# Kernel optimization log

Hardware: AMD Instinct MI355X
Metric: run time of the kernel (lower is better)

Reference implementation:

```python
import jax, jax.numpy as jnp
import numpy as np

D, FF, E, K = 1024, 1024, 8, 2  # d_model, ffn_dim, n_experts, top_k
B, S = 4, 1024


def _gelu(x):
    # torch F.gelu default is the exact erf form
    return jax.nn.gelu(x, approximate=False)


def setup_inputs() -> dict:
    key = jax.random.key(0)
    ks = jax.random.split(key, 12)
    s = 0.02
    return {
        "x": jax.random.normal(ks[0], (B, S, D), jnp.float32),
        "gate_w": jax.random.normal(ks[1], (D, E), jnp.float32) * s,
        "gate_b": jnp.zeros((E,), jnp.float32),
        # shared expert (n_shared = 1)
        "sw1": jax.random.normal(ks[2], (D, FF), jnp.float32) * s,
        "sb1": jnp.zeros((FF,), jnp.float32),
        "sw2": jax.random.normal(ks[3], (FF, D), jnp.float32) * s,
        "sb2": jnp.zeros((D,), jnp.float32),
        # routed experts, stacked over E
        "w1": jax.random.normal(ks[4], (E, D, FF), jnp.float32) * s,
        "b1": jnp.zeros((E, FF), jnp.float32),
        "w2": jax.random.normal(ks[5], (E, FF, D), jnp.float32) * s,
        "b2": jnp.zeros((E, D), jnp.float32),
    }


def reference(x, gate_w, gate_b, sw1, sb1, sw2, sb2, w1, b1, w2, b2):
    Bb, Ss, Dm = x.shape
    t = x.reshape(-1, Dm)  # [T, D]
    T = t.shape[0]

    # shared expert(s)
    shared = _gelu(t @ sw1 + sb1) @ sw2 + sb2  # [T, D]

    # gating: softmax over experts, then top-k
    probs = jax.nn.softmax(t @ gate_w + gate_b, axis=-1)  # [T, E]
    topk_p, topk_i = jax.lax.top_k(probs, K)  # [T, K]

    # combine weights: sparse [T, E] with top-k probs (top_k indices are distinct)
    combine = jnp.zeros((T, E), t.dtype).at[
        jnp.arange(T)[:, None], topk_i
    ].set(topk_p)

    # expert FFNs computed densely, combined with sparse routing weights;
    # mathematically identical to the masked gather-GEMM-scatter loop
    h = _gelu(jnp.einsum("td,edf->etf", t, w1) + b1[:, None, :])  # [E, T, FF]
    y = jnp.einsum("etf,efd->etd", h, w2) + b2[:, None, :]        # [E, T, D]
    routed = jnp.einsum("te,etd->td", combine, y)                  # [T, D]

    return (routed + shared).reshape(Bb, Ss, Dm)
```

## Files before the change

### kernel.cpp

```cpp
#include <hip/hip_runtime.h>
#include <hip/hip_bf16.h>


typedef short short8 __attribute__((ext_vector_type(8)));
typedef float f32x4  __attribute__((ext_vector_type(4)));

#define T_TOK 4096
#define NSLOT 8192

#define OFF_XB    (size_t)0
#define OFF_W1T   (size_t)8388608
#define OFF_W2T   (size_t)25165824
#define OFF_SW1T  (size_t)41943040
#define OFF_SW2T  (size_t)44040192
#define OFF_HS    (size_t)46137344
#define OFF_HR    (size_t)54525952
#define OFF_META  (size_t)73400320
#define OFF_ROWMAP (size_t)73400576
#define OFF_ROWW  (size_t)73437440
#define OFF_TKI   (size_t)73474304
#define OFF_TKP   (size_t)73507072

__device__ __forceinline__ unsigned short f2bf(float f) {
  __hip_bfloat16 h = __float2bfloat16(f);
  return __builtin_bit_cast(unsigned short, h);
}
__device__ __forceinline__ float gelu_exact(float x) {
  return 0.5f * x * (1.0f + erff(x * 0.70710678118654752f));
}

#define GLOAD16(g, l)                                                          \
  __builtin_amdgcn_global_load_lds(                                            \
      (const __attribute__((address_space(1))) void*)(g),                      \
      (__attribute__((address_space(3))) void*)(l), 16, 0, 0)


__global__ void k_transpose(const float* __restrict__ w1, const float* __restrict__ w2,
                            const float* __restrict__ sw1, const float* __restrict__ sw2,
                            unsigned short* __restrict__ w1t, unsigned short* __restrict__ w2t,
                            unsigned short* __restrict__ sw1t, unsigned short* __restrict__ sw2t) {
  __shared__ float tile[32][33];
  int z = blockIdx.z;
  const float* src; unsigned short* dst;
  if (z < 8)       { src = w1 + (size_t)z * 1048576;        dst = w1t + (size_t)z * 1048576; }
  else if (z < 16) { src = w2 + (size_t)(z - 8) * 1048576;  dst = w2t + (size_t)(z - 8) * 1048576; }
  else if (z == 16){ src = sw1; dst = sw1t; }
  else             { src = sw2; dst = sw2t; }
  int tx = threadIdx.x, ty = threadIdx.y;
  int gx = blockIdx.x * 32 + tx;
#pragma unroll
  for (int j = 0; j < 4; j++) {
    int gy = blockIdx.y * 32 + ty + j * 8;
    tile[ty + j * 8][tx] = src[(size_t)gy * 1024 + gx];
  }
  __syncthreads();
#pragma unroll
  for (int j = 0; j < 4; j++) {
    int orow = blockIdx.x * 32 + ty + j * 8;
    int ocol = blockIdx.y * 32 + tx;
    dst[(size_t)orow * 1024 + ocol] = f2bf(tile[tx][ty + j * 8]);
  }
}

__global__ void k_convert_x(const float* __restrict__ x, unsigned short* __restrict__ xb) {
  int i = blockIdx.x * blockDim.x + threadIdx.x;
  float4 v = ((const float4*)x)[i];
  ushort4 o;
  o.x = f2bf(v.x); o.y = f2bf(v.y); o.z = f2bf(v.z); o.w = f2bf(v.w);
  ((ushort4*)xb)[i] = o;
}

__global__ void k_gate(const float* __restrict__ x, const float* __restrict__ gw,
                       const float* __restrict__ gb, int* __restrict__ tki,
                       float* __restrict__ tkp) {
  int wv = threadIdx.x >> 6, l = threadIdx.x & 63;
  int t = blockIdx.x * 4 + wv;
  float acc[8] = {0, 0, 0, 0, 0, 0, 0, 0};
  const float* xr = x + (size_t)t * 1024;
#pragma unroll
  for (int j = 0; j < 16; j++) {
    int k = j * 64 + l;
    float xv = xr[k];
    const float4* g4 = (const float4*)(gw + (size_t)k * 8);
    float4 ga = g4[0], gbv = g4[1];
    acc[0] += xv * ga.x; acc[1] += xv * ga.y; acc[2] += xv * ga.z; acc[3] += xv * ga.w;
    acc[4] += xv * gbv.x; acc[5] += xv * gbv.y; acc[6] += xv * gbv.z; acc[7] += xv * gbv.w;
  }
#pragma unroll
  for (int off = 32; off > 0; off >>= 1) {
#pragma unroll
    for (int e = 0; e < 8; e++) acc[e] += __shfl_xor(acc[e], off);
  }
  if (l == 0) {
    float lg[8], p[8];
    float m = -1e30f;
#pragma unroll
    for (int e = 0; e < 8; e++) { lg[e] = acc[e] + gb[e]; m = fmaxf(m, lg[e]); }
    float s = 0.f;
#pragma unroll
    for (int e = 0; e < 8; e++) { p[e] = expf(lg[e] - m); s += p[e]; }
    float inv = 1.0f / s;
#pragma unroll
    for (int e = 0; e < 8; e++) p[e] *= inv;
    int i0 = 0;
#pragma unroll
    for (int e = 1; e < 8; e++) if (p[e] > p[i0]) i0 = e;
    int i1 = (i0 == 0) ? 1 : 0;
#pragma unroll
    for (int e = 0; e < 8; e++) if (e != i0 && p[e] > p[i1]) i1 = e;
    tki[t * 2] = i0; tki[t * 2 + 1] = i1;
    tkp[t * 2] = p[i0]; tkp[t * 2 + 1] = p[i1];
  }
}

__global__ void k_route(const int* __restrict__ tki, const float* __restrict__ tkp,
                        int* __restrict__ counts, int* __restrict__ basev,
                        int* __restrict__ rowmap, float* __restrict__ roww) {
  int e = blockIdx.x, tid = threadIdx.x;
  int lane = tid & 63, wv = tid >> 6;
  int c[8] = {0, 0, 0, 0, 0, 0, 0, 0};
  for (int i = tid; i < NSLOT; i += 256) {
    int v = tki[i];
#pragma unroll
    for (int q = 0; q < 8; q++) c[q] += (v == q);
  }
  __shared__ int red[8][64];
#pragma unroll
  for (int q = 0; q < 8; q++) {
#pragma unroll
    for (int off = 32; off > 0; off >>= 1) c[q] += __shfl_xor(c[q], off);
  }
  if (lane == 0) {
#pragma unroll
    for (int q = 0; q < 8; q++) red[q][wv] = c[q];
  }
  __syncthreads();
  __shared__ int cnt_s[8], base_s[8];
  if (tid == 0) {
    int off = 0;
#pragma unroll
    for (int q = 0; q < 8; q++) {
      int cq = red[q][0] + red[q][1] + red[q][2] + red[q][3];
      cnt_s[q] = cq; base_s[q] = off;
      off += (cq + 127) & ~127;
    }
    counts[e] = cnt_s[e];
    basev[e] = base_s[e];
  }
  __syncthreads();
  __shared__ int warpsum[4];
  int wpos = base_s[e];
  for (int i0 = 0; i0 < NSLOT; i0 += 256) {
    int i = i0 + tid;
    bool pred = (tki[i] == e);
    unsigned long long mask = __ballot(pred);
    int wpre = __popcll(mask & ((1ull << lane) - 1));
    if (lane == 0) warpsum[wv] = __popcll(mask);
    __syncthreads();
    int wbase = 0;
    for (int w = 0; w < wv; w++) wbase += warpsum[w];
    int total = warpsum[0] + warpsum[1] + warpsum[2] + warpsum[3];
    if (pred) {
      int pos = wpos + wbase + wpre;
      rowmap[pos] = i >> 1;
      roww[pos] = tkp[i];
    }
    wpos += total;
    __syncthreads();
  }
}

template <int PHASE>
__global__ __launch_bounds__(256, 4) void k_ffn(
    const unsigned short* __restrict__ As,
    const unsigned short* __restrict__ Ar,
    const unsigned short* __restrict__ Bsh, const float* __restrict__ bsh,
    const unsigned short* __restrict__ Brt, const float* __restrict__ brt,
    unsigned short* __restrict__ Hsh, unsigned short* __restrict__ Hrt,
    float* __restrict__ outf,
    const int* __restrict__ rowmap, const float* __restrict__ roww,
    const int* __restrict__ counts, const int* __restrict__ bases) {
  __shared__ unsigned short ldsA[128 * 64];
  __shared__ unsigned short ldsB[128 * 64];

  int z = blockIdx.z;
  int row0 = blockIdx.y * 128;
  int nrows, rbase = 0;
  const unsigned short* Bmat;
  const float* bvec;
  const unsigned short* Amat;
  if (z == 0) {
    nrows = T_TOK;
    if (row0 >= nrows) return;
    Bmat = Bsh; bvec = bsh; Amat = As;
  } else {
    int e = z - 1;
    nrows = counts[e]; rbase = bases[e];
    if (row0 >= nrows) return;
    Bmat = Brt + (size_t)e * 1048576;
    bvec = brt + (size_t)e * 1024;
    Amat = (PHASE == 1) ? As : Ar;
  }
  int n0 = blockIdx.x * 128;
  int tid = threadIdx.x, wave = tid >> 6, lane = tid & 63;
  int wm = wave >> 1, wn = wave & 1;

  long arow[4];
#pragma unroll
  for (int i = 0; i < 4; i++) {
    int q = i * 4 + wave;
    int m = (q * 64 + lane) >> 3;
    int r = row0 + m;
    if (r >= nrows) r = nrows - 1;
    if (z == 0)            arow[i] = r;
    else if (PHASE == 1)   arow[i] = rowmap[rbase + r];
    else                   arow[i] = rbase + r;
  }

  f32x4 acc[4][4];
#pragma unroll
  for (int i = 0; i < 4; i++)
#pragma unroll
    for (int j = 0; j < 4; j++) acc[i][j] = (f32x4){0.f, 0.f, 0.f, 0.f};

  for (int k0 = 0; k0 < 1024; k0 += 64) {
#pragma unroll
    for (int i = 0; i < 4; i++) {
      int q = i * 4 + wave;
      int c = q * 64 + lane;
      int m = c >> 3, s = c & 7;
      int ks = s ^ (m & 7);
      GLOAD16(Amat + arow[i] * 1024 + k0 + ks * 8, &ldsA[q * 512]);
    }
#pragma unroll
    for (int i = 0; i < 4; i++) {
      int q = i * 4 + wave;
      int c = q * 64 + lane;
      int n = c >> 3, s = c & 7;
      int ks = s ^ (n & 7);
      GLOAD16(Bmat + (size_t)(n0 + n) * 1024 + k0 + ks * 8, &ldsB[q * 512]);
    }
    __syncthreads();
#pragma unroll
    for (int kk = 0; kk < 2; kk++) {
      short8 af[4], bfr[4];
      int kc0 = kk * 4 + (lane >> 4);
#pragma unroll
      for (int fi = 0; fi < 4; fi++) {
        int m = wm * 64 + fi * 16 + (lane & 15);
        int slot = kc0 ^ (m & 7);
        af[fi] = *(const short8*)&ldsA[m * 64 + slot * 8];
      }
#pragma unroll
      for (int fj = 0; fj < 4; fj++) {
        int n = wn * 64 + fj * 16 + (lane & 15);
        int slot = kc0 ^ (n & 7);
        bfr[fj] = *(const short8*)&ldsB[n * 64 + slot * 8];
      }
#pragma unroll
      for (int fi = 0; fi < 4; fi++)
#pragma unroll
        for (int fj = 0; fj < 4; fj++)
          acc[fi][fj] = __builtin_amdgcn_mfma_f32_16x16x32_bf16(af[fi], bfr[fj], acc[fi][fj], 0, 0, 0);
    }
    __syncthreads();
  }

#pragma unroll
  for (int fi = 0; fi < 4; fi++) {
#pragma unroll
    for (int rg = 0; rg < 4; rg++) {
      int lr = wm * 64 + fi * 16 + (lane >> 4) * 4 + rg;
      int r = row0 + lr;
      if (r >= nrows) continue;
      if (PHASE == 1) {
        unsigned short* dst = (z == 0) ? (Hsh + (size_t)r * 1024)
                                       : (Hrt + (size_t)(rbase + r) * 1024);
#pragma unroll
        for (int fj = 0; fj < 4; fj++) {
          int col = n0 + wn * 64 + fj * 16 + (lane & 15);
          dst[col] = f2bf(gelu_exact(acc[fi][fj][rg] + bvec[col]));
        }
      } else {
        if (z == 0) {
#pragma unroll
          for (int fj = 0; fj < 4; fj++) {
            int col = n0 + wn * 64 + fj * 16 + (lane & 15);
            atomicAdd(&outf[(size_t)r * 1024 + col], acc[fi][fj][rg] + bvec[col]);
          }
        } else {
          int tok = rowmap[rbase + r];
          float p = roww[rbase + r];
#pragma unroll
          for (int fj = 0; fj < 4; fj++) {
            int col = n0 + wn * 64 + fj * 16 + (lane & 15);
            atomicAdd(&outf[(size_t)tok * 1024 + col], p * (acc[fi][fj][rg] + bvec[col]));
          }
        }
      }
    }
  }
}

extern "C" void kernel_launch(void* const* d_in, const int* in_sizes, int n_in,
                              void* d_out, int out_size, void* d_ws, size_t ws_size,
                              hipStream_t stream) {
  const float* x   = (const float*)d_in[0];
  const float* gw  = (const float*)d_in[1];
  const float* gb  = (const float*)d_in[2];
  const float* sw1 = (const float*)d_in[3];
  const float* sb1 = (const float*)d_in[4];
  const float* sw2 = (const float*)d_in[5];
  const float* sb2 = (const float*)d_in[6];
  const float* w1  = (const float*)d_in[7];
  const float* b1  = (const float*)d_in[8];
  const float* w2  = (const float*)d_in[9];
  const float* b2  = (const float*)d_in[10];
  float* out = (float*)d_out;
  char* ws = (char*)d_ws;

  unsigned short* xb   = (unsigned short*)(ws + OFF_XB);
  unsigned short* w1t  = (unsigned short*)(ws + OFF_W1T);
  unsigned short* w2t  = (unsigned short*)(ws + OFF_W2T);
  unsigned short* sw1t = (unsigned short*)(ws + OFF_SW1T);
  unsigned short* sw2t = (unsigned short*)(ws + OFF_SW2T);
  unsigned short* Hs   = (unsigned short*)(ws + OFF_HS);
  unsigned short* Hr   = (unsigned short*)(ws + OFF_HR);
  int*   counts = (int*)(ws + OFF_META);
  int*   basev  = counts + 8;
  int*   rowmap = (int*)(ws + OFF_ROWMAP);
  float* roww   = (float*)(ws + OFF_ROWW);
  int*   tki    = (int*)(ws + OFF_TKI);
  float* tkp    = (float*)(ws + OFF_TKP);

  hipMemsetAsync(out, 0, (size_t)out_size * sizeof(float), stream);
  k_transpose<<<dim3(32, 32, 18), dim3(32, 8), 0, stream>>>(w1, w2, sw1, sw2, w1t, w2t, sw1t, sw2t);
  k_convert_x<<<4096, 256, 0, stream>>>(x, xb);
  k_gate<<<1024, 256, 0, stream>>>(x, gw, gb, tki, tkp);
  k_route<<<8, 256, 0, stream>>>(tki, tkp, counts, basev, rowmap, roww);

  k_ffn<1><<<dim3(8, 64, 9), 256, 0, stream>>>(xb, xb, sw1t, sb1, w1t, b1, Hs, Hr,
                                               nullptr, rowmap, roww, counts, basev);
  k_ffn<2><<<dim3(8, 64, 9), 256, 0, stream>>>(Hs, Hr, sw2t, sb2, w2t, b2, nullptr, nullptr,
                                               out, rowmap, roww, counts, basev);
}
```

Before: 192.8 us.

## Double-buffer LDS tiles and compact FFN grid into a flat tile list

Adds double-buffered LDS staging so global loads for the next K tile are issued while MFMAs run on the current one. This drops one barrier per iteration, and launch bounds fall to 2 waves per EU to fit the doubled LDS. It also swaps the 8x64x9 grid, which held many early-exiting empty blocks, for a flat 832-workgroup launch. Each block derives its (expert, row tile, column tile) from the routing counts, and the blocks are interleaved across 8 groups. The grid size assumes the total tile count never exceeds 832; that holds because 8192 routed slots give at most 72 routed row tiles, and with the 32 shared row tiles that is at most 104 x 8 = 832.

```diff
diff --git a/kernel.cpp b/kernel.cpp
--- a/kernel.cpp
+++ b/kernel.cpp
@@ -7,6 +7,8 @@
 
 #define T_TOK 4096
 #define NSLOT 8192
+#define NWG   832
+#define CHUNK 104
 
 #define OFF_XB    (size_t)0
 #define OFF_W1T   (size_t)8388608
@@ -170,8 +172,27 @@
   }
 }
 
+#define STAGE_TILE(buf, kk0)                                                   \
+  {                                                                            \
+    _Pragma("unroll") for (int i = 0; i < 4; i++) {                            \
+      int q = i * 4 + wave;                                                    \
+      int c = q * 64 + lane;                                                   \
+      int m = c >> 3, s = c & 7;                                               \
+      int ks = s ^ (m & 7);                                                    \
+      GLOAD16(Amat + arow[i] * 1024 + (kk0) + ks * 8, &ldsA[buf][q * 512]);    \
+    }                                                                          \
+    _Pragma("unroll") for (int i = 0; i < 4; i++) {                            \
+      int q = i * 4 + wave;                                                    \
+      int c = q * 64 + lane;                                                   \
+      int n = c >> 3, s = c & 7;                                               \
+      int ks = s ^ (n & 7);                                                    \
+      GLOAD16(Bmat + (size_t)(n0 + n) * 1024 + (kk0) + ks * 8,                 \
+              &ldsB[buf][q * 512]);                                            \
+    }                                                                          \
+  }
+
 template <int PHASE>
-__global__ __launch_bounds__(256, 4) void k_ffn(
+__global__ __launch_bounds__(256, 2) void k_ffn(
     const unsigned short* __restrict__ As,
     const unsigned short* __restrict__ Ar,
     const unsigned short* __restrict__ Bsh, const float* __restrict__ bsh,
@@ -180,28 +201,39 @@
     float* __restrict__ outf,
     const int* __restrict__ rowmap, const float* __restrict__ roww,
     const int* __restrict__ counts, const int* __restrict__ bases) {
-  __shared__ unsigned short ldsA[128 * 64];
-  __shared__ unsigned short ldsB[128 * 64];
-
-  int z = blockIdx.z;
-  int row0 = blockIdx.y * 128;
+  __shared__ unsigned short ldsA[2][128 * 64];
+  __shared__ unsigned short ldsB[2][128 * 64];
+
+  int bid = blockIdx.x;
+  int j = (bid & 7) * CHUNK + (bid >> 3);
+  int z = -1, rel = j;
+  if (rel < 256) {
+    z = 0;
+  } else {
+    rel -= 256;
+#pragma unroll
+    for (int e = 0; e < 8; e++) {
+      int nye = ((counts[e] + 127) >> 7) << 3;
+      if (z < 0) {
+        if (rel < nye) z = e + 1; else rel -= nye;
+      }
+    }
+    if (z < 0) return;
+  }
+  int row0 = (rel >> 3) * 128;
+  int n0 = (rel & 7) * 128;
+
   int nrows, rbase = 0;
-  const unsigned short* Bmat;
-  const float* bvec;
-  const unsigned short* Amat;
+  const unsigned short* Bmat; const float* bvec; const unsigned short* Amat;
   if (z == 0) {
-    nrows = T_TOK;
-    if (row0 >= nrows) return;
-    Bmat = Bsh; bvec = bsh; Amat = As;
+    nrows = T_TOK; Bmat = Bsh; bvec = bsh; Amat = As;
   } else {
     int e = z - 1;
     nrows = counts[e]; rbase = bases[e];
-    if (row0 >= nrows) return;
     Bmat = Brt + (size_t)e * 1048576;
     bvec = brt + (size_t)e * 1024;
     Amat = (PHASE == 1) ? As : Ar;
   }
-  int n0 = blockIdx.x * 128;
   int tid = threadIdx.x, wave = tid >> 6, lane = tid & 63;
   int wm = wave >> 1, wn = wave & 1;
 
@@ -221,26 +253,15 @@
 #pragma unroll
   for (int i = 0; i < 4; i++)
 #pragma unroll
-    for (int j = 0; j < 4; j++) acc[i][j] = (f32x4){0.f, 0.f, 0.f, 0.f};
-
-  for (int k0 = 0; k0 < 1024; k0 += 64) {
-#pragma unroll
-    for (int i = 0; i < 4; i++) {
-      int q = i * 4 + wave;
-      int c = q * 64 + lane;
-      int m = c >> 3, s = c & 7;
-      int ks = s ^ (m & 7);
-      GLOAD16(Amat + arow[i] * 1024 + k0 + ks * 8, &ldsA[q * 512]);
-    }
-#pragma unroll
-    for (int i = 0; i < 4; i++) {
-      int q = i * 4 + wave;
-      int c = q * 64 + lane;
-      int n = c >> 3, s = c & 7;
-      int ks = s ^ (n & 7);
-      GLOAD16(Bmat + (size_t)(n0 + n) * 1024 + k0 + ks * 8, &ldsB[q * 512]);
-    }
-    __syncthreads();
+    for (int j2 = 0; j2 < 4; j2++) acc[i][j2] = (f32x4){0.f, 0.f, 0.f, 0.f};
+
+  STAGE_TILE(0, 0);
+  __syncthreads();
+
+#pragma unroll 2
+  for (int t = 0; t < 16; ++t) {
+    int b = t & 1;
+    if (t < 15) STAGE_TILE(b ^ 1, (t + 1) * 64);
 #pragma unroll
     for (int kk = 0; kk < 2; kk++) {
       short8 af[4], bfr[4];
@@ -249,13 +270,13 @@
       for (int fi = 0; fi < 4; fi++) {
         int m = wm * 64 + fi * 16 + (lane & 15);
         int slot = kc0 ^ (m & 7);
-        af[fi] = *(const short8*)&ldsA[m * 64 + slot * 8];
+        af[fi] = *(const short8*)&ldsA[b][m * 64 + slot * 8];
       }
 #pragma unroll
       for (int fj = 0; fj < 4; fj++) {
         int n = wn * 64 + fj * 16 + (lane & 15);
         int slot = kc0 ^ (n & 7);
-        bfr[fj] = *(const short8*)&ldsB[n * 64 + slot * 8];
+        bfr[fj] = *(const short8*)&ldsB[b][n * 64 + slot * 8];
       }
 #pragma unroll
       for (int fi = 0; fi < 4; fi++)
@@ -339,8 +360,8 @@
   k_gate<<<1024, 256, 0, stream>>>(x, gw, gb, tki, tkp);
   k_route<<<8, 256, 0, stream>>>(tki, tkp, counts, basev, rowmap, roww);
 
-  k_ffn<1><<<dim3(8, 64, 9), 256, 0, stream>>>(xb, xb, sw1t, sb1, w1t, b1, Hs, Hr,
-                                               nullptr, rowmap, roww, counts, basev);
-  k_ffn<2><<<dim3(8, 64, 9), 256, 0, stream>>>(Hs, Hr, sw2t, sb2, w2t, b2, nullptr, nullptr,
-                                               out, rowmap, roww, counts, basev);
-}
+  k_ffn<1><<<NWG, 256, 0, stream>>>(xb, xb, sw1t, sb1, w1t, b1, Hs, Hr,
+                                    nullptr, rowmap, roww, counts, basev);
+  k_ffn<2><<<NWG, 256, 0, stream>>>(Hs, Hr, sw2t, sb2, w2t, b2, nullptr, nullptr,
+                                    out, rowmap, roww, counts, basev);
+}
```

After: 223.4 us. 1.16x slower.
